# Kernel optimization log

Hardware: AMD Instinct MI355X
Metric: run time of the kernel (lower is better)

## Reference

```python
import jax, jax.numpy as jnp
import numpy as np

DIM = 1024
HEADS = 16
DIM_HEAD = 64
INNER = HEADS * DIM_HEAD  # 1024


def xnorm(t, gamma):
    # t * gamma / ||t||_2 along last dim (keepdims)
    norm = jnp.linalg.norm(t, ord=2, axis=-1, keepdims=True)
    return t * gamma / norm


def setup_inputs() -> dict:
    key = jax.random.key(0)
    k0, k1, k2, k3, k4 = jax.random.split(key, 5)
    x = jax.random.normal(k0, (4, 4096, DIM), dtype=jnp.float32)
    # nn.Linear weights init with std=0.001, biases zero (per init_weights)
    W_qkv = jax.random.normal(k1, (DIM, 3 * INNER), dtype=jnp.float32) * 0.001
    W_o = jax.random.normal(k2, (INNER, DIM), dtype=jnp.float32) * 0.001
    b_o = jnp.zeros((DIM,), dtype=jnp.float32)
    gamma = jax.random.normal(k3, (1, HEADS, 1, 1), dtype=jnp.float32)
    return {"x": x, "W_qkv": W_qkv, "W_o": W_o, "b_o": b_o, "gamma": gamma}


def reference(x, W_qkv, W_o, b_o, gamma):
    b, n, _ = x.shape
    qkv = x @ W_qkv  # [b, n, 3*inner]
    q, k, v = jnp.split(qkv, 3, axis=-1)
    # [b, n, h*d] -> [b, h, n, d]
    reshape_heads = lambda t: t.reshape(b, n, HEADS, DIM_HEAD).transpose(0, 2, 1, 3)
    q, k, v = map(reshape_heads, (q, k, v))
    # kv = k^T v : [b, h, d, d]
    kv = jnp.einsum('bhnd,bhne->bhde', k, v)
    kv_n = xnorm(kv, gamma)
    q_n = xnorm(q, gamma)
    out = jnp.einsum('bhnd,bhde->bhne', q_n, kv_n)  # [b, h, n, d]
    out = out.transpose(0, 2, 1, 3).reshape(b, n, INNER)
    return out @ W_o + b_o
```

## Files before the change

kernel.cpp:

```cpp
#include <hip/hip_runtime.h>


typedef __bf16 bf16;
typedef bf16  bf16x8 __attribute__((ext_vector_type(8)));
typedef bf16  bf16x4 __attribute__((ext_vector_type(4)));
typedef float f32x4  __attribute__((ext_vector_type(4)));

#define BATCH   4
#define SEQ     4096
#define DIM     1024
#define HEADS   16
#define DHEAD   64
#define MTOK    (BATCH*SEQ)
#define N_QKV   (3*DIM)
#define NSPLIT  16

#define NB_PACK (MTOK*DIM/(8*256))
#define NB_T1   ((N_QKV/32)*(DIM/32))
#define NB_T2   ((DIM/32)*(DIM/32))

typedef __attribute__((address_space(1))) const void gas_v;
typedef __attribute__((address_space(3))) void las_v;

__device__ __forceinline__ void gld_lds16(const void* g, void* l) {
  __builtin_amdgcn_global_load_lds((gas_v*)g, (las_v*)l, 16, 0, 0);
}

template <int VMN>
__device__ __forceinline__ void vmwait() {
  if constexpr (VMN == 8)      asm volatile("s_waitcnt vmcnt(8)" ::: "memory");
  else if constexpr (VMN == 4) asm volatile("s_waitcnt vmcnt(4)" ::: "memory");
  else if constexpr (VMN == 0) asm volatile("s_waitcnt vmcnt(0)" ::: "memory");
}

#define PH_BAR() __builtin_amdgcn_s_barrier()

__global__ __launch_bounds__(256) void prep(const float* __restrict__ x,
                                            const float* __restrict__ Wqkv,
                                            const float* __restrict__ Wo,
                                            bf16* __restrict__ xb,
                                            bf16* __restrict__ WqT,
                                            bf16* __restrict__ WoT) {
  const int bid = blockIdx.x;
  const int t   = threadIdx.x;
  if (bid < NB_PACK) {
    size_t i = (size_t)bid * 256 + t;
    f32x4 a = *(const f32x4*)&x[i * 8];
    f32x4 b = *(const f32x4*)&x[i * 8 + 4];
    bf16x8 o = {(bf16)a.x, (bf16)a.y, (bf16)a.z, (bf16)a.w,
                (bf16)b.x, (bf16)b.y, (bf16)b.z, (bf16)b.w};
    *(bf16x8*)&xb[i * 8] = o;
    return;
  }
  __shared__ float tile[32][33];
  const float* in; bf16* out; int R, C, bx, by;
  if (bid < NB_PACK + NB_T1) {
    int tid = bid - NB_PACK;
    in = Wqkv; out = WqT; R = DIM; C = N_QKV;
    bx = tid % (N_QKV / 32); by = tid / (N_QKV / 32);
  } else {
    int tid = bid - NB_PACK - NB_T1;
    in = Wo; out = WoT; R = DIM; C = DIM;
    bx = tid & 31; by = tid >> 5;
  }
  int c0 = bx * 32, r0 = by * 32;
  int tx = t & 31, ty = t >> 5;
#pragma unroll
  for (int i = 0; i < 32; i += 8)
    tile[ty + i][tx] = in[(size_t)(r0 + ty + i) * C + c0 + tx];
  __syncthreads();
#pragma unroll
  for (int i = 0; i < 32; i += 8)
    out[(size_t)(c0 + ty + i) * R + r0 + tx] = (bf16)tile[tx][ty + i];
}

template <int MODE>
__global__ __launch_bounds__(512) void gemm256(
    const bf16* __restrict__ A, const bf16* __restrict__ Bt, int N, int K,
    float* __restrict__ C, const float* __restrict__ bias,
    const float* __restrict__ gamma,
    bf16* __restrict__ qn, bf16* __restrict__ kb, bf16* __restrict__ vb) {
  __shared__ bf16 lds[4][2][256 * 32];
  const int t    = threadIdx.x;
  const int lane = t & 63;
  const int wv   = t >> 6;
  const int wr   = wv >> 2;
  const int wc   = wv & 3;

  const int GX  = gridDim.x;
  const int nwg = GX * gridDim.y;
  int lin = blockIdx.y * GX + blockIdx.x;
  lin = (lin & 7) * (nwg >> 3) + (lin >> 3);
  const int m0 = (lin / GX) * 256;
  const int n0 = (lin % GX) * 256;

  const int lr   = lane & 15;
  const int ks   = lane >> 4;

  if (MODE == 2) Bt += (size_t)(m0 >> 12) * DIM * DIM;

  int aoff[8], boff[4];
#pragma unroll
  for (int i = 0; i < 8; i++) {
    int ra  = wr * 128 + i * 16 + lr;
    aoff[i] = ra * 32 + ((ks ^ ((ra >> 1) & 3)) * 8);
  }
#pragma unroll
  for (int j = 0; j < 4; j++) {
    int rb  = wc * 64 + j * 16 + lr;
    boff[j] = rb * 32 + ((ks ^ ((rb >> 1) & 3)) * 8);
  }

  const int srow = t >> 2;
  const int sseg = t & 3;

  const bf16* Asrc = A;
  const bf16* Bsrc = Bt;
  auto stage = [&](int half, int bufi, int tt) {
    const bf16* src = half ? Bsrc : Asrc;
    const int   rb0 = half ? n0 : m0;
    const int   k0  = tt << 5;
#pragma unroll
    for (int p = 0; p < 2; ++p) {
      int row  = p * 128 + srow;
      int gseg = sseg ^ ((row >> 1) & 3);
      gld_lds16(src + (size_t)(rb0 + row) * K + k0 + gseg * 8,
                &lds[bufi][half][row * 32 + sseg * 8]);
    }
  };

  f32x4 acc[8][4];
#pragma unroll
  for (int i = 0; i < 8; i++)
#pragma unroll
    for (int j = 0; j < 4; j++) acc[i][j] = {0.f, 0.f, 0.f, 0.f};

#define TILE(BUFI, DOSTAGE, STT, VM)                                          \
  {                                                                           \
    const int bb = (BUFI);                                                    \
    bf16x8 bfv[4], af[4];                                                     \
    _Pragma("unroll") for (int j = 0; j < 4; j++)                             \
        bfv[j] = *(const bf16x8*)&lds[bb][1][boff[j]];                        \
    _Pragma("unroll") for (int i = 0; i < 4; i++)                             \
        af[i] = *(const bf16x8*)&lds[bb][0][aoff[i]];                         \
    if (DOSTAGE) stage(0, (STT) & 3, (STT));                                  \
    PH_BAR();                                                                 \
    __builtin_amdgcn_s_setprio(1);                                            \
    _Pragma("unroll") for (int i = 0; i < 4; i++)                             \
        _Pragma("unroll") for (int j = 0; j < 4; j++)                         \
            acc[i][j] = __builtin_amdgcn_mfma_f32_16x16x32_bf16(              \
                af[i], bfv[j], acc[i][j], 0, 0, 0);                           \
    __builtin_amdgcn_s_setprio(0);                                            \
    PH_BAR();                                                                 \
    _Pragma("unroll") for (int i = 0; i < 4; i++)                             \
        af[i] = *(const bf16x8*)&lds[bb][0][aoff[4 + i]];                     \
    if (DOSTAGE) stage(1, (STT) & 3, (STT));                                  \
    vmwait<VM>();                                                             \
    PH_BAR();                                                                 \
    __builtin_amdgcn_s_setprio(1);                                            \
    _Pragma("unroll") for (int i = 0; i < 4; i++)                             \
        _Pragma("unroll") for (int j = 0; j < 4; j++)                         \
            acc[4 + i][j] = __builtin_amdgcn_mfma_f32_16x16x32_bf16(          \
                af[i], bfv[j], acc[4 + i][j], 0, 0, 0);                       \
    __builtin_amdgcn_s_setprio(0);                                            \
    PH_BAR();                                                                 \
  }

  const int NT = K >> 5;
  stage(0, 0, 0); stage(1, 0, 0);
  stage(0, 1, 1); stage(1, 1, 1);
  stage(0, 2, 2); stage(1, 2, 2);
  asm volatile("s_waitcnt vmcnt(8)" ::: "memory");
  PH_BAR();

  for (int tt = 0; tt < NT - 3; ++tt) TILE(tt & 3, true, tt + 3, 8);
  TILE((NT - 3) & 3, false, 0, 4);
  TILE((NT - 2) & 3, false, 0, 0);
  TILE((NT - 1) & 3, false, 0, -1);
#undef TILE

  const int crow0 = m0 + wr * 128 + (lane >> 4) * 4;

  if (MODE == 2) {
    const int ccol0 = n0 + wc * 64 + lr;
#pragma unroll
    for (int i = 0; i < 8; i++)
#pragma unroll
      for (int j = 0; j < 4; j++) {
        int col = ccol0 + j * 16;
#pragma unroll
        for (int r = 0; r < 4; r++)
          C[(size_t)(crow0 + i * 16 + r) * N + col] = acc[i][j][r] + bias[col];
      }
  } else {
    const int seg = n0 >> 10;
    if (seg == 0) {
      const int h    = (n0 + wc * 64) >> 6;
      const float g  = gamma[h];
      const int col0 = n0 + wc * 64 + lr;
#pragma unroll
      for (int i = 0; i < 8; i++)
#pragma unroll
        for (int r = 0; r < 4; r++) {
          float p = acc[i][0][r] * acc[i][0][r] + acc[i][1][r] * acc[i][1][r]
                  + acc[i][2][r] * acc[i][2][r] + acc[i][3][r] * acc[i][3][r];
          p += __shfl_xor(p, 1);
          p += __shfl_xor(p, 2);
          p += __shfl_xor(p, 4);
          p += __shfl_xor(p, 8);
          float sc = g * rsqrtf(p);
          size_t rb = (size_t)(crow0 + i * 16 + r) * DIM + col0;
#pragma unroll
          for (int j = 0; j < 4; j++)
            qn[rb + j * 16] = (bf16)(acc[i][j][r] * sc);
        }
    } else {
      bf16* dst = (seg == 1) ? kb : vb;
      const int ccol0 = (n0 - (seg << 10)) + wc * 64 + lr;
#pragma unroll
      for (int i = 0; i < 8; i++)
#pragma unroll
        for (int j = 0; j < 4; j++) {
          int col = ccol0 + j * 16;
#pragma unroll
          for (int r = 0; r < 4; r++)
            dst[(size_t)(crow0 + i * 16 + r) * DIM + col] = (bf16)acc[i][j][r];
        }
    }
  }
}

__global__ __launch_bounds__(256) void kv_partial(const bf16* __restrict__ kb,
                                                  const bf16* __restrict__ vb,
                                                  float* __restrict__ part) {
  __shared__ float lK[32 * 64];
  __shared__ float lV[32 * 64];
  const int t  = threadIdx.x;
  const int s  = blockIdx.x;
  const int bh = blockIdx.y;
  const int b  = bh >> 4, h = bh & 15;
  const size_t base = ((size_t)b * SEQ + s * (SEQ / NSPLIT)) * DIM + h * DHEAD;
  const int d0 = (t & 15) * 4, e0 = (t >> 4) * 4;
  const int rr = t >> 3, cc = (t & 7) * 8;

  float acc[4][4];
#pragma unroll
  for (int a = 0; a < 4; a++)
#pragma unroll
    for (int q = 0; q < 4; q++) acc[a][q] = 0.f;

  for (int nt = 0; nt < (SEQ / NSPLIT) / 32; nt++) {
    size_t g = base + (size_t)(nt * 32 + rr) * DIM + cc;
    bf16x8 k8 = *(const bf16x8*)(kb + g);
    bf16x8 v8 = *(const bf16x8*)(vb + g);
    f32x4 klo = {(float)k8[0], (float)k8[1], (float)k8[2], (float)k8[3]};
    f32x4 khi = {(float)k8[4], (float)k8[5], (float)k8[6], (float)k8[7]};
    f32x4 vlo = {(float)v8[0], (float)v8[1], (float)v8[2], (float)v8[3]};
    f32x4 vhi = {(float)v8[4], (float)v8[5], (float)v8[6], (float)v8[7]};
    *(f32x4*)&lK[rr * 64 + cc]     = klo;
    *(f32x4*)&lK[rr * 64 + cc + 4] = khi;
    *(f32x4*)&lV[rr * 64 + cc]     = vlo;
    *(f32x4*)&lV[rr * 64 + cc + 4] = vhi;
    __syncthreads();
#pragma unroll 8
    for (int nn = 0; nn < 32; nn++) {
      f32x4 kk = *(const f32x4*)&lK[nn * 64 + d0];
      f32x4 vv = *(const f32x4*)&lV[nn * 64 + e0];
#pragma unroll
      for (int a = 0; a < 4; a++)
#pragma unroll
        for (int q = 0; q < 4; q++) acc[a][q] += kk[a] * vv[q];
    }
    __syncthreads();
  }
  float* pb = part + ((size_t)bh * NSPLIT + s) * 4096;
#pragma unroll
  for (int a = 0; a < 4; a++) {
    f32x4 o = {acc[a][0], acc[a][1], acc[a][2], acc[a][3]};
    *(f32x4*)&pb[(d0 + a) * 64 + e0] = o;
  }
}

__global__ __launch_bounds__(256) void kv_norm(const float* __restrict__ part,
                                               const float* __restrict__ gamma,
                                               bf16* __restrict__ kvn) {
  const int t   = threadIdx.x;
  const int bh  = blockIdx.x >> 2;
  const int h   = bh & 15;
  const int d   = (blockIdx.x & 3) * 16 + (t >> 4);
  const int e0  = (t & 15) * 4;
  f32x4 v = {0.f, 0.f, 0.f, 0.f};
  for (int s = 0; s < NSPLIT; s++) {
    f32x4 a = *(const f32x4*)(part + ((size_t)bh * NSPLIT + s) * 4096 + d * 64 + e0);
    v.x += a.x; v.y += a.y; v.z += a.z; v.w += a.w;
  }
  float ss = v.x * v.x + v.y * v.y + v.z * v.z + v.w * v.w;
  ss += __shfl_xor(ss, 1);
  ss += __shfl_xor(ss, 2);
  ss += __shfl_xor(ss, 4);
  ss += __shfl_xor(ss, 8);
  float scale = gamma[h] * rsqrtf(ss);
  bf16x4 o = {(bf16)(v.x * scale), (bf16)(v.y * scale),
              (bf16)(v.z * scale), (bf16)(v.w * scale)};
  *(bf16x4*)&kvn[(size_t)bh * 4096 + d * 64 + e0] = o;
}

__global__ __launch_bounds__(256) void mfold(const bf16* __restrict__ WoT,
                                             const bf16* __restrict__ kvn,
                                             bf16* __restrict__ Mt) {
  __shared__ bf16 lA[128 * 64];
  __shared__ bf16 lB[64 * 64];
  const int t    = threadIdx.x;
  const int lane = t & 63;
  const int wv   = t >> 6;
  const int bh   = blockIdx.y;
  const int b    = bh >> 4, h = bh & 15;
  const int n0   = blockIdx.x * 128;

#pragma unroll
  for (int p = 0; p < 4; p++) {
    int c = p * 256 + t;
    int row = c >> 3, seg = c & 7;
    int gsk = seg ^ (row & 7);
    gld_lds16(WoT + (size_t)(n0 + row) * DIM + h * 64 + gsk * 8,
              &lA[row * 64 + seg * 8]);
  }
#pragma unroll
  for (int p = 0; p < 2; p++) {
    int c = p * 256 + t;
    int row = c >> 3, seg = c & 7;
    int gsk = seg ^ (row & 7);
    gld_lds16(kvn + (size_t)bh * 4096 + row * 64 + gsk * 8,
              &lB[row * 64 + seg * 8]);
  }
  __syncthreads();

  const int lr = lane & 15, ks = lane >> 4;
  f32x4 acc[2][4];
#pragma unroll
  for (int i = 0; i < 2; i++)
#pragma unroll
    for (int j = 0; j < 4; j++) acc[i][j] = {0.f, 0.f, 0.f, 0.f};

#pragma unroll
  for (int kk = 0; kk < 2; kk++) {
    bf16x8 af[2], bkv[4];
#pragma unroll
    for (int i = 0; i < 2; i++) {
      int row = wv * 32 + i * 16 + lr;
      int seg = (kk * 4 + ks) ^ (row & 7);
      af[i] = *(const bf16x8*)&lA[row * 64 + seg * 8];
    }
#pragma unroll
    for (int j = 0; j < 4; j++) {
      int row = j * 16 + lr;
      int seg = (kk * 4 + ks) ^ (row & 7);
      bkv[j] = *(const bf16x8*)&lB[row * 64 + seg * 8];
    }
#pragma unroll
    for (int i = 0; i < 2; i++)
#pragma unroll
      for (int j = 0; j < 4; j++)
        acc[i][j] = __builtin_amdgcn_mfma_f32_16x16x32_bf16(af[i], bkv[j],
                                                            acc[i][j], 0, 0, 0);
  }

  bf16* mb = Mt + (size_t)b * DIM * DIM;
#pragma unroll
  for (int i = 0; i < 2; i++)
#pragma unroll
    for (int j = 0; j < 4; j++) {
      int col = h * 64 + j * 16 + lr;
#pragma unroll
      for (int r = 0; r < 4; r++) {
        int row = n0 + wv * 32 + i * 16 + ks * 4 + r;
        mb[(size_t)row * DIM + col] = (bf16)acc[i][j][r];
      }
    }
}

extern "C" void kernel_launch(void* const* d_in, const int* in_sizes, int n_in,
                              void* d_out, int out_size, void* d_ws,
                              size_t ws_size, hipStream_t stream) {
  const float* x     = (const float*)d_in[0];
  const float* Wqkv  = (const float*)d_in[1];
  const float* Wo    = (const float*)d_in[2];
  const float* bo    = (const float*)d_in[3];
  const float* gamma = (const float*)d_in[4];
  float* out = (float*)d_out;

  char* ws = (char*)d_ws;
  size_t off = 0;
  bf16*  xb   = (bf16*)(ws + off);  off += (size_t)MTOK * DIM * 2;
  bf16*  WqT  = (bf16*)(ws + off);  off += (size_t)N_QKV * DIM * 2;
  bf16*  WoT  = (bf16*)(ws + off);  off += (size_t)DIM * DIM * 2;
  bf16*  kvn  = (bf16*)(ws + off);  off += (size_t)64 * 4096 * 2;
  bf16*  qn   = (bf16*)(ws + off);  off += (size_t)MTOK * DIM * 2;
  bf16*  kb   = (bf16*)(ws + off);  off += (size_t)MTOK * DIM * 2;
  bf16*  vb   = (bf16*)(ws + off);  off += (size_t)MTOK * DIM * 2;
  float* part = (float*)(ws + off); off += (size_t)64 * NSPLIT * 4096 * 4;
  bf16*  Mt   = (bf16*)(ws + off);  off += (size_t)BATCH * DIM * DIM * 2;

  prep<<<dim3(NB_PACK + NB_T1 + NB_T2), dim3(256), 0, stream>>>(
      x, Wqkv, Wo, xb, WqT, WoT);

  gemm256<1><<<dim3(N_QKV / 256, MTOK / 256), dim3(512), 0, stream>>>(
      xb, WqT, N_QKV, DIM, nullptr, nullptr, gamma, qn, kb, vb);

  kv_partial<<<dim3(NSPLIT, 64), dim3(256), 0, stream>>>(kb, vb, part);
  kv_norm<<<dim3(256), dim3(256), 0, stream>>>(part, gamma, kvn);

  mfold<<<dim3(DIM / 128, 64), dim3(256), 0, stream>>>(WoT, kvn, Mt);

  gemm256<2><<<dim3(DIM / 256, MTOK / 256), dim3(512), 0, stream>>>(
      qn, Mt, DIM, DIM, out, bo, nullptr, nullptr, nullptr, nullptr);
}
```

Before: 318.1 us.

## Restructure GEMM main loop into double-buffered 64-wide K tiles with fewer barriers

Replaces the four-slot ring of 32-wide K tiles, which used four barriers per tile, with a two-slot double buffer. Each slot holds two 32-wide slices, so one iteration covers 64 of K, and each slice gets one barrier plus one vmcnt wait. The B fragments are loaded once per slice and the A and B loads for the next tile are issued between MFMA phases. This is meant to cut barrier and wait overhead, at the cost of a shallower prefetch distance that may expose more global-load latency.

Result: no change. 318.8 us (+0.2%).

```diff
diff --git a/kernel.cpp b/kernel.cpp
--- a/kernel.cpp
+++ b/kernel.cpp
@@ -28,8 +28,7 @@
 
 template <int VMN>
 __device__ __forceinline__ void vmwait() {
-  if constexpr (VMN == 8)      asm volatile("s_waitcnt vmcnt(8)" ::: "memory");
-  else if constexpr (VMN == 4) asm volatile("s_waitcnt vmcnt(4)" ::: "memory");
+  if constexpr (VMN == 4) asm volatile("s_waitcnt vmcnt(4)" ::: "memory");
   else if constexpr (VMN == 0) asm volatile("s_waitcnt vmcnt(0)" ::: "memory");
 }
 
@@ -80,7 +79,7 @@
     float* __restrict__ C, const float* __restrict__ bias,
     const float* __restrict__ gamma,
     bf16* __restrict__ qn, bf16* __restrict__ kb, bf16* __restrict__ vb) {
-  __shared__ bf16 lds[4][2][256 * 32];
+  __shared__ bf16 lds[2][2][2][256 * 32];
   const int t    = threadIdx.x;
   const int lane = t & 63;
   const int wv   = t >> 6;
@@ -111,21 +110,18 @@
     boff[j] = rb * 32 + ((ks ^ ((rb >> 1) & 3)) * 8);
   }
 
-  const int srow = t >> 2;
-  const int sseg = t & 3;
-
   const bf16* Asrc = A;
   const bf16* Bsrc = Bt;
-  auto stage = [&](int half, int bufi, int tt) {
-    const bf16* src = half ? Bsrc : Asrc;
-    const int   rb0 = half ? n0 : m0;
-    const int   k0  = tt << 5;
+  auto stage = [&](int op, int sl, int bufi, int tt) {
+    const bf16* src = op ? Bsrc : Asrc;
+    const int   rb0 = op ? n0 : m0;
+    const int   k0  = tt * 64 + sl * 32;
 #pragma unroll
     for (int p = 0; p < 2; ++p) {
-      int row  = p * 128 + srow;
-      int gseg = sseg ^ ((row >> 1) & 3);
+      int row  = p * 128 + (t >> 2);
+      int gseg = (t & 3) ^ ((row >> 1) & 3);
       gld_lds16(src + (size_t)(rb0 + row) * K + k0 + gseg * 8,
-                &lds[bufi][half][row * 32 + sseg * 8]);
+                &lds[bufi][op][sl][row * 32 + (t & 3) * 8]);
     }
   };
 
@@ -135,49 +131,54 @@
 #pragma unroll
     for (int j = 0; j < 4; j++) acc[i][j] = {0.f, 0.f, 0.f, 0.f};
 
-#define TILE(BUFI, DOSTAGE, STT, VM)                                          \
+  bf16x8 af[4], bfv[4];
+
+#define PHASE(IBASE, READB, SL, BB, DOST, SOP, SSL, STT)                      \
   {                                                                           \
-    const int bb = (BUFI);                                                    \
-    bf16x8 bfv[4], af[4];                                                     \
-    _Pragma("unroll") for (int j = 0; j < 4; j++)                             \
-        bfv[j] = *(const bf16x8*)&lds[bb][1][boff[j]];                        \
+    const bf16* sA = &lds[BB][0][SL][0];                                      \
+    const bf16* sB = &lds[BB][1][SL][0];                                      \
+    if (READB) {                                                              \
+      _Pragma("unroll") for (int j = 0; j < 4; j++)                           \
+          bfv[j] = *(const bf16x8*)&sB[boff[j]];                              \
+    }                                                                         \
     _Pragma("unroll") for (int i = 0; i < 4; i++)                             \
-        af[i] = *(const bf16x8*)&lds[bb][0][aoff[i]];                         \
-    if (DOSTAGE) stage(0, (STT) & 3, (STT));                                  \
-    PH_BAR();                                                                 \
+        af[i] = *(const bf16x8*)&sA[aoff[(IBASE) + i]];                       \
+    if (DOST) stage(SOP, SSL, (BB) ^ 1, STT);                                 \
     __builtin_amdgcn_s_setprio(1);                                            \
     _Pragma("unroll") for (int i = 0; i < 4; i++)                             \
-        _Pragma("unroll") for (int j = 0; j < 4; j++)                         \
-            acc[i][j] = __builtin_amdgcn_mfma_f32_16x16x32_bf16(              \
-                af[i], bfv[j], acc[i][j], 0, 0, 0);                           \
+      _Pragma("unroll") for (int j = 0; j < 4; j++)                           \
+          acc[(IBASE) + i][j] = __builtin_amdgcn_mfma_f32_16x16x32_bf16(      \
+              af[i], bfv[j], acc[(IBASE) + i][j], 0, 0, 0);                   \
     __builtin_amdgcn_s_setprio(0);                                            \
-    PH_BAR();                                                                 \
-    _Pragma("unroll") for (int i = 0; i < 4; i++)                             \
-        af[i] = *(const bf16x8*)&lds[bb][0][aoff[4 + i]];                     \
-    if (DOSTAGE) stage(1, (STT) & 3, (STT));                                  \
-    vmwait<VM>();                                                             \
-    PH_BAR();                                                                 \
-    __builtin_amdgcn_s_setprio(1);                                            \
-    _Pragma("unroll") for (int i = 0; i < 4; i++)                             \
-        _Pragma("unroll") for (int j = 0; j < 4; j++)                         \
-            acc[4 + i][j] = __builtin_amdgcn_mfma_f32_16x16x32_bf16(          \
-                af[i], bfv[j], acc[4 + i][j], 0, 0, 0);                       \
-    __builtin_amdgcn_s_setprio(0);                                            \
-    PH_BAR();                                                                 \
-  }
-
-  const int NT = K >> 5;
-  stage(0, 0, 0); stage(1, 0, 0);
-  stage(0, 1, 1); stage(1, 1, 1);
-  stage(0, 2, 2); stage(1, 2, 2);
-  asm volatile("s_waitcnt vmcnt(8)" ::: "memory");
+  }
+
+  const int NT = K >> 6;
+  stage(0, 0, 0, 0); stage(1, 0, 0, 0);
+  stage(0, 1, 0, 0); stage(1, 1, 0, 0);
+  vmwait<4>();
   PH_BAR();
 
-  for (int tt = 0; tt < NT - 3; ++tt) TILE(tt & 3, true, tt + 3, 8);
-  TILE((NT - 3) & 3, false, 0, 4);
-  TILE((NT - 2) & 3, false, 0, 0);
-  TILE((NT - 1) & 3, false, 0, -1);
-#undef TILE
+  for (int tt = 0; tt < NT - 1; ++tt) {
+    const int bb = tt & 1;
+    PHASE(0, 1, 0, bb, 1, 0, 0, tt + 1);
+    PHASE(4, 0, 0, bb, 1, 1, 0, tt + 1);
+    vmwait<4>();
+    PH_BAR();
+    PHASE(0, 1, 1, bb, 1, 0, 1, tt + 1);
+    PHASE(4, 0, 1, bb, 1, 1, 1, tt + 1);
+    vmwait<4>();
+    PH_BAR();
+  }
+  {
+    const int bb = (NT - 1) & 1;
+    PHASE(0, 1, 0, bb, 0, 0, 0, 0);
+    PHASE(4, 0, 0, bb, 0, 0, 0, 0);
+    vmwait<0>();
+    PH_BAR();
+    PHASE(0, 1, 1, bb, 0, 0, 0, 0);
+    PHASE(4, 0, 1, bb, 0, 0, 0, 0);
+  }
+#undef PHASE
 
   const int crow0 = m0 + wr * 128 + (lane >> 4) * 4;
 
```
